# Optimization experiments

Measured on AMD Instinct MI355X. Metric: run time of the kernel, lower is better.

The kernel has to match this reference:

```python
import jax, jax.numpy as jnp
import numpy as np

N, IN_SZ, OUT_SZ = 8192, 512, 64

def setup_inputs() -> dict:
    key = jax.random.key(0)
    ks = jax.random.split(key, 7)
    s_in = 1.0 / np.sqrt(IN_SZ)
    inp = {
        "input": jax.random.normal(ks[0], (N, IN_SZ), dtype=jnp.float32),
        "Wq": jax.random.uniform(ks[1], (OUT_SZ, IN_SZ), jnp.float32, -s_in, s_in),
        "bq": jax.random.uniform(ks[2], (OUT_SZ,), jnp.float32, -s_in, s_in),
        "Wk": jax.random.uniform(ks[3], (OUT_SZ, IN_SZ), jnp.float32, -s_in, s_in),
        "bk": jax.random.uniform(ks[4], (OUT_SZ,), jnp.float32, -s_in, s_in),
        "Wv": jax.random.uniform(ks[5], (OUT_SZ, IN_SZ), jnp.float32, -s_in, s_in),
        "bv": jax.random.uniform(ks[6], (OUT_SZ,), jnp.float32, -s_in, s_in),
    }
    return inp

def reference(input, Wq, bq, Wk, bk, Wv, bv):
    # torch nn.Linear: x @ W.T + b
    q = input @ Wq.T + bq  # [N, out]
    k = input @ Wk.T + bk  # [N, out]
    v = input @ Wv.T + bv  # [N, out]
    # NOTE: original module has NO 1/sqrt(d) scaling.
    scores = jax.nn.softmax(q @ k.T, axis=-1)  # [N, N]
    return scores @ v  # [N, out]
```

## Files before the change

### kernel.cpp

```cpp
#include <hip/hip_runtime.h>
#include <math.h>

#define SA_N   8192
#define SA_IN  512
#define SA_D   64
#define G_SPL  16
#define LOG2E  1.44269504f

typedef short s16x8 __attribute__((ext_vector_type(8)));
typedef float f32x16 __attribute__((ext_vector_type(16)));

#define MFMA32(A, B, C) __builtin_amdgcn_mfma_f32_32x32x16_bf16((A), (B), (C), 0, 0, 0)

static __device__ __forceinline__ unsigned short f2bf_rn(float x) {
    unsigned int u = __float_as_uint(x);
    unsigned int r = (u + 0x7FFFu + ((u >> 16) & 1u)) >> 16;
    return (unsigned short)r;
}

static __device__ __forceinline__ void trunc_split(float f, unsigned short* hi, unsigned short* lo) {
    unsigned int u = __float_as_uint(f);
    *hi = (unsigned short)(u >> 16);
    float lf = f - __uint_as_float(u & 0xFFFF0000u);
    *lo = (unsigned short)(__float_as_uint(lf) >> 16);
}

static __device__ __forceinline__ unsigned int pack_hi16(unsigned int u0, unsigned int u1) {
    return __builtin_amdgcn_perm(u1, u0, 0x07060302u);
}

static __device__ __forceinline__ void split8(const float4 a, const float4 b, s16x8* xh, s16x8* xl) {
    union { unsigned int u[4]; s16x8 v; } H, L;
    const float f[8] = {a.x, a.y, a.z, a.w, b.x, b.y, b.z, b.w};
#pragma unroll
    for (int p = 0; p < 4; ++p) {
        const unsigned int u0 = __float_as_uint(f[2 * p]);
        const unsigned int u1 = __float_as_uint(f[2 * p + 1]);
        H.u[p] = pack_hi16(u0, u1);
        const float l0 = f[2 * p]     - __uint_as_float(u0 & 0xFFFF0000u);
        const float l1 = f[2 * p + 1] - __uint_as_float(u1 & 0xFFFF0000u);
        L.u[p] = pack_hi16(__float_as_uint(l0), __float_as_uint(l1));
    }
    *xh = H.v; *xl = L.v;
}

__global__ __launch_bounds__(256) void prep_w_kernel(
    const float* __restrict__ Wq, const float* __restrict__ Wk, const float* __restrict__ Wv,
    unsigned short* __restrict__ WqH, unsigned short* __restrict__ WqL,
    unsigned short* __restrict__ WkH, unsigned short* __restrict__ WkL,
    unsigned short* __restrict__ WvR)
{
    const int i   = blockIdx.x * 256 + threadIdx.x;
    const int mat = i >> 13;
    const int j   = i & 8191;
    const float4 v = (mat == 0 ? (const float4*)Wq
                    : mat == 1 ? (const float4*)Wk
                               : (const float4*)Wv)[j];
    const float f[4] = {v.x, v.y, v.z, v.w};
    if (mat < 2) {
        unsigned short hs[4], ls[4];
#pragma unroll
        for (int e = 0; e < 4; ++e) trunc_split(f[e], &hs[e], &ls[e]);
        ushort4 H = {hs[0], hs[1], hs[2], hs[3]};
        ushort4 L = {ls[0], ls[1], ls[2], ls[3]};
        unsigned short* WH = mat ? WkH : WqH;
        unsigned short* WL = mat ? WkL : WqL;
        *(ushort4*)(WH + (size_t)j * 4) = H;
        *(ushort4*)(WL + (size_t)j * 4) = L;
    } else {
        ushort4 R = {f2bf_rn(f[0]), f2bf_rn(f[1]), f2bf_rn(f[2]), f2bf_rn(f[3])};
        *(ushort4*)(WvR + (size_t)j * 4) = R;
    }
}

__global__ __launch_bounds__(256, 2) void qkv_kernel(
    const float* __restrict__ in,
    const unsigned short* __restrict__ WqH, const unsigned short* __restrict__ WqL,
    const unsigned short* __restrict__ WkH, const unsigned short* __restrict__ WkL,
    const unsigned short* __restrict__ WvR,
    const float* __restrict__ bq, const float* __restrict__ bk, const float* __restrict__ bv,
    unsigned short* __restrict__ Qhi, unsigned short* __restrict__ Qlo,
    unsigned short* __restrict__ KhiF, unsigned short* __restrict__ VF)
{
    __shared__ float cbuf[2][4][64][20];
    __shared__ __align__(16) unsigned short stage[4096];
    const int t    = threadIdx.x;
    const int w    = t >> 6;
    const int lane = t & 63;
    const int h    = lane >> 5;
    const int q32  = lane & 31;
    const int mat  = blockIdx.x >> 8;
    const int jt   = blockIdx.x & 255;
    const int rows0 = jt * 32;

    const unsigned short* WH = (mat == 0) ? WqH : (mat == 1 ? WkH : WvR);
    const unsigned short* WL = (mat == 0) ? WqL : WkL;
    const float* B = (mat == 0) ? bq : (mat == 1 ? bk : bv);

    f32x16 accA[2] = {};
    f32x16 accB[2] = {};

#pragma unroll 2
    for (int ksl = 0; ksl < 8; ++ksl) {
        const int ks = (w << 3) + ksl;
        const float* xp = in + (size_t)(rows0 + q32) * SA_IN + ks * 16 + h * 8;
        const float4 xa = *(const float4*)xp;
        const float4 xb = *(const float4*)(xp + 4);
        s16x8 xh, xl;
        split8(xa, xb, &xh, &xl);
#pragma unroll
        for (int mt = 0; mt < 2; ++mt) {
            const size_t woff = (size_t)(mt * 32 + q32) * SA_IN + ks * 16 + h * 8;
            const s16x8 ah = *(const s16x8*)(WH + woff);
            if (mat < 2) {
                const s16x8 al = *(const s16x8*)(WL + woff);
                accA[mt] = MFMA32(ah, xh, accA[mt]);
                accB[mt] = MFMA32(ah, xl, accB[mt]);
                accA[mt] = MFMA32(al, xh, accA[mt]);
            } else {
                accA[mt] = MFMA32(ah, xh, accA[mt]);
            }
        }
    }

#pragma unroll
    for (int mt = 0; mt < 2; ++mt) {
        f32x16 tot = accA[mt];
        if (mat < 2) {
#pragma unroll
            for (int r = 0; r < 16; ++r) tot[r] += accB[mt][r];
        }
#pragma unroll
        for (int rg = 0; rg < 4; ++rg) {
            float4 vv = { tot[4 * rg + 0], tot[4 * rg + 1],
                          tot[4 * rg + 2], tot[4 * rg + 3] };
            *(float4*)&cbuf[mt][w][lane][4 * rg] = vv;
        }
    }
    __syncthreads();
    if (w < 2) {
        const int mt = w;
        float c[16];
#pragma unroll
        for (int rg = 0; rg < 4; ++rg) {
            const float4 s0 = *(const float4*)&cbuf[mt][0][lane][4 * rg];
            const float4 s1 = *(const float4*)&cbuf[mt][1][lane][4 * rg];
            const float4 s2 = *(const float4*)&cbuf[mt][2][lane][4 * rg];
            const float4 s3 = *(const float4*)&cbuf[mt][3][lane][4 * rg];
            c[4 * rg + 0] = (s0.x + s1.x) + (s2.x + s3.x);
            c[4 * rg + 1] = (s0.y + s1.y) + (s2.y + s3.y);
            c[4 * rg + 2] = (s0.z + s1.z) + (s2.z + s3.z);
            c[4 * rg + 3] = (s0.w + s1.w) + (s2.w + s3.w);
        }
#pragma unroll
        for (int r = 0; r < 16; ++r) {
            const int o = mt * 32 + (r & 3) + 8 * (r >> 2) + 4 * h;
            float val = c[r] + B[o];
            if (mat == 0) {
                val *= LOG2E;
                unsigned short hi, lo;
                trunc_split(val, &hi, &lo);
                stage[q32 * 64 + o]        = hi;
                stage[2048 + q32 * 64 + o] = lo;
            } else if (mat == 1) {
                const int kl_ = ((o >> 4) * 64 + ((o >> 3) & 1) * 32 + q32) * 8 + (o & 7);
                stage[kl_] = f2bf_rn(val);
            } else {
                const int hp = (q32 >> 2) & 1;
                const int ip = (q32 & 3) + ((q32 >> 3) & 1) * 4;
                const int vl_ = ((o >> 5) * 2 + (q32 >> 4)) * 512
                              + hp * 256 + (o & 31) * 8 + ip;
                stage[vl_] = f2bf_rn(val);
            }
        }
    }
    __syncthreads();

    {
        const uint4* st4 = (const uint4*)stage;
        if (mat == 0) {
            for (int i = t; i < 512; i += 256) {
                unsigned short* dst = ((i < 256) ? Qhi : Qlo) + (size_t)rows0 * 64 + (i & 255) * 8;
                *(uint4*)dst = st4[i];
            }
        } else if (mat == 1) {
            if (t < 256) *(uint4*)(KhiF + (size_t)jt * 2048 + t * 8) = st4[t];
        } else {
            *(uint4*)(VF + (size_t)jt * 2048 + t * 8) = st4[t];
        }
    }
}

__global__ __launch_bounds__(512, 2) void attn_kernel(
    const unsigned short* __restrict__ Qhi, const unsigned short* __restrict__ Qlo,
    const unsigned short* __restrict__ KhiF, const unsigned short* __restrict__ VF,
    unsigned short* __restrict__ Opart, float* __restrict__ Lpart)
{
    __shared__ __align__(16) unsigned short kbuf[2][2][2048];
    const int t    = threadIdx.x;
    const int w    = t >> 6;
    const int lane = t & 63;
    const int h    = lane >> 5;
    const int q32  = lane & 31;
    const int qb   = blockIdx.x >> 4;
    const int g    = blockIdx.x & 15;
    const int q0   = (qb * 8 + w) * 32;
    const int jt0  = g * 16;

    const int half = t >> 8;
    const int ti   = t & 255;

    s16x8 qh[4], ql[4];
#pragma unroll
    for (int s = 0; s < 4; ++s) {
        const size_t off = (size_t)(q0 + q32) * 64 + s * 16 + h * 8;
        qh[s] = *reinterpret_cast<const s16x8*>(Qhi + off);
        ql[s] = *reinterpret_cast<const s16x8*>(Qlo + off);
    }

    const unsigned short* SRC = half ? VF : KhiF;

    {
        const uint4 a = *(const uint4*)(SRC + (size_t)jt0 * 2048 + ti * 8);
        *(uint4*)&kbuf[0][half][ti * 8] = a;
    }
    __syncthreads();

    f32x16 O0 = {}, O1 = {};
    float lsum = 0.f;

    for (int it = 0; it < 16; ++it) {
        const int p = it & 1;

        uint4 na;
        if (it < 15) {
            na = *(const uint4*)(SRC + (size_t)(jt0 + it + 1) * 2048 + ti * 8);
        }

        s16x8 kh[4], vv[4];
#pragma unroll
        for (int s = 0; s < 4; ++s) {
            kh[s] = *(const s16x8*)&kbuf[p][0][(s * 64 + lane) * 8];
            vv[s] = *(const s16x8*)&kbuf[p][1][(s * 64 + lane) * 8];
        }

        f32x16 Sa = {}, Sb = {};
        __builtin_amdgcn_s_setprio(1);
#pragma unroll
        for (int s = 0; s < 4; ++s) {
            Sa = MFMA32(kh[s], qh[s], Sa);
            Sb = MFMA32(kh[s], ql[s], Sb);
        }
        __builtin_amdgcn_s_setprio(0);

        float e[16];
#pragma unroll
        for (int r = 0; r < 16; ++r) e[r] = __builtin_amdgcn_exp2f(Sa[r] + Sb[r]);
        lsum += (((e[0] + e[1]) + (e[2] + e[3])) + ((e[4] + e[5]) + (e[6] + e[7])))
              + (((e[8] + e[9]) + (e[10] + e[11])) + ((e[12] + e[13]) + (e[14] + e[15])));

        union { unsigned int u[4]; s16x8 v; } P0, P1;
#pragma unroll
        for (int j2 = 0; j2 < 4; ++j2) {
            P0.u[j2] = pack_hi16(__float_as_uint(e[2 * j2]),     __float_as_uint(e[2 * j2 + 1]));
            P1.u[j2] = pack_hi16(__float_as_uint(e[8 + 2 * j2]), __float_as_uint(e[8 + 2 * j2 + 1]));
        }

        __builtin_amdgcn_s_setprio(1);
        O0 = MFMA32(vv[0], P0.v, O0);
        O0 = MFMA32(vv[1], P1.v, O0);
        O1 = MFMA32(vv[2], P0.v, O1);
        O1 = MFMA32(vv[3], P1.v, O1);
        __builtin_amdgcn_s_setprio(0);

        if (it < 15) {
            *(uint4*)&kbuf[1 - p][half][ti * 8] = na;
        }
        __syncthreads();
    }

    lsum += __shfl_xor(lsum, 32, 64);

    const size_t qg = (size_t)g * SA_N + q0 + q32;
#pragma unroll
    for (int rg = 0; rg < 4; ++rg) {
        const int d0 = 8 * rg + 4 * h;
        uint2 s0, s1;
        s0.x = (unsigned int)f2bf_rn(O0[4 * rg + 0]) | ((unsigned int)f2bf_rn(O0[4 * rg + 1]) << 16);
        s0.y = (unsigned int)f2bf_rn(O0[4 * rg + 2]) | ((unsigned int)f2bf_rn(O0[4 * rg + 3]) << 16);
        s1.x = (unsigned int)f2bf_rn(O1[4 * rg + 0]) | ((unsigned int)f2bf_rn(O1[4 * rg + 1]) << 16);
        s1.y = (unsigned int)f2bf_rn(O1[4 * rg + 2]) | ((unsigned int)f2bf_rn(O1[4 * rg + 3]) << 16);
        *(uint2*)(Opart + qg * 64 + d0)      = s0;
        *(uint2*)(Opart + qg * 64 + d0 + 32) = s1;
    }
    if (h == 0) Lpart[qg] = lsum;
}

__global__ __launch_bounds__(256) void combine_kernel(
    const unsigned short* __restrict__ Opart, const float* __restrict__ Lpart,
    float* __restrict__ out)
{
    const int tid = blockIdx.x * 256 + threadIdx.x;
    const int q  = tid >> 5;
    const int dp = tid & 31;
    const unsigned int* OP = (const unsigned int*)Opart;
    float s0 = 0.f, s1 = 0.f, lt = 0.f;
#pragma unroll
    for (int g = 0; g < G_SPL; ++g) {
        const unsigned int v = OP[((size_t)g * SA_N + q) * 32 + dp];
        s0 += __uint_as_float(v << 16);
        s1 += __uint_as_float(v & 0xFFFF0000u);
        lt += Lpart[(size_t)g * SA_N + q];
    }
    float2 r = { s0 / lt, s1 / lt };
    *(float2*)&out[(size_t)q * 64 + dp * 2] = r;
}

extern "C" void kernel_launch(void* const* d_in, const int* in_sizes, int n_in,
                              void* d_out, int out_size, void* d_ws, size_t ws_size,
                              hipStream_t stream) {
    const float* input = (const float*)d_in[0];
    const float* Wq    = (const float*)d_in[1];
    const float* bq    = (const float*)d_in[2];
    const float* Wk    = (const float*)d_in[3];
    const float* bk    = (const float*)d_in[4];
    const float* Wv    = (const float*)d_in[5];
    const float* bv    = (const float*)d_in[6];
    float* out = (float*)d_out;

    const size_t SEG = (size_t)SA_N * 64;
    unsigned short* Qhi  = (unsigned short*)d_ws;
    unsigned short* Qlo  = Qhi  + SEG;
    unsigned short* KhiF = Qlo  + SEG;
    unsigned short* VF   = KhiF + SEG;
    unsigned short* Opart = VF  + SEG;
    float*          Lpart = (float*)(Opart + (size_t)G_SPL * SA_N * 64);
    unsigned short* WqH = (unsigned short*)(Lpart + (size_t)G_SPL * SA_N);
    unsigned short* WqL = WqH + 32768;
    unsigned short* WkH = WqL + 32768;
    unsigned short* WkL = WkH + 32768;
    unsigned short* WvR = WkL + 32768;

    prep_w_kernel<<<96, 256, 0, stream>>>(Wq, Wk, Wv, WqH, WqL, WkH, WkL, WvR);
    qkv_kernel<<<768, 256, 0, stream>>>(input, WqH, WqL, WkH, WkL, WvR,
                                        bq, bk, bv, Qhi, Qlo, KhiF, VF);
    attn_kernel<<<32 * G_SPL, 512, 0, stream>>>(Qhi, Qlo, KhiF, VF, Opart, Lpart);
    combine_kernel<<<1024, 256, 0, stream>>>(Opart, Lpart, out);
}
```

Measured before the change: 128.2 us.

## Pre-split input to bf16 hi/lo once and retile QKV projection to 64-row tiles

The input matrix is now converted to bf16 hi/lo halves once in the prep kernel and written to workspace, so the QKV kernel no longer re-reads fp32 input and re-splits it for each of the three matrices. The QKV kernel is retiled so each block covers 64 rows, with each wave owning one 32x32 output tile over the full K dimension. This removes the cross-wave split-K reduction through shared memory and one barrier. In exchange it adds a full write and read of an 8 MB split-input buffer, halves the QKV grid, and gives each wave a longer serial K loop.

Result: slower. 140.8 us (+9.8%).

```diff
diff --git a/kernel.cpp b/kernel.cpp
--- a/kernel.cpp
+++ b/kernel.cpp
@@ -29,52 +29,56 @@
     return __builtin_amdgcn_perm(u1, u0, 0x07060302u);
 }
 
-static __device__ __forceinline__ void split8(const float4 a, const float4 b, s16x8* xh, s16x8* xl) {
-    union { unsigned int u[4]; s16x8 v; } H, L;
-    const float f[8] = {a.x, a.y, a.z, a.w, b.x, b.y, b.z, b.w};
-#pragma unroll
-    for (int p = 0; p < 4; ++p) {
-        const unsigned int u0 = __float_as_uint(f[2 * p]);
-        const unsigned int u1 = __float_as_uint(f[2 * p + 1]);
-        H.u[p] = pack_hi16(u0, u1);
-        const float l0 = f[2 * p]     - __uint_as_float(u0 & 0xFFFF0000u);
-        const float l1 = f[2 * p + 1] - __uint_as_float(u1 & 0xFFFF0000u);
-        L.u[p] = pack_hi16(__float_as_uint(l0), __float_as_uint(l1));
-    }
-    *xh = H.v; *xl = L.v;
-}
-
-__global__ __launch_bounds__(256) void prep_w_kernel(
+__global__ __launch_bounds__(256) void prep_kernel(
+    const float* __restrict__ in,
     const float* __restrict__ Wq, const float* __restrict__ Wk, const float* __restrict__ Wv,
+    unsigned short* __restrict__ Xhi, unsigned short* __restrict__ Xlo,
     unsigned short* __restrict__ WqH, unsigned short* __restrict__ WqL,
     unsigned short* __restrict__ WkH, unsigned short* __restrict__ WkL,
     unsigned short* __restrict__ WvR)
 {
-    const int i   = blockIdx.x * 256 + threadIdx.x;
-    const int mat = i >> 13;
-    const int j   = i & 8191;
-    const float4 v = (mat == 0 ? (const float4*)Wq
-                    : mat == 1 ? (const float4*)Wk
-                               : (const float4*)Wv)[j];
-    const float f[4] = {v.x, v.y, v.z, v.w};
-    if (mat < 2) {
-        unsigned short hs[4], ls[4];
-#pragma unroll
-        for (int e = 0; e < 4; ++e) trunc_split(f[e], &hs[e], &ls[e]);
-        ushort4 H = {hs[0], hs[1], hs[2], hs[3]};
-        ushort4 L = {ls[0], ls[1], ls[2], ls[3]};
-        unsigned short* WH = mat ? WkH : WqH;
-        unsigned short* WL = mat ? WkL : WqL;
-        *(ushort4*)(WH + (size_t)j * 4) = H;
-        *(ushort4*)(WL + (size_t)j * 4) = L;
+    const int b = blockIdx.x;
+    if (b < 1024) {
+        const int base = (b * 256 + threadIdx.x) * 4;
+        const float4* src = (const float4*)in;
+#pragma unroll
+        for (int j = 0; j < 4; ++j) {
+            const float4 v = src[base + j];
+            ushort4 H, L;
+            trunc_split(v.x, &H.x, &L.x);
+            trunc_split(v.y, &H.y, &L.y);
+            trunc_split(v.z, &H.z, &L.z);
+            trunc_split(v.w, &H.w, &L.w);
+            ((ushort4*)Xhi)[base + j] = H;
+            ((ushort4*)Xlo)[base + j] = L;
+        }
     } else {
-        ushort4 R = {f2bf_rn(f[0]), f2bf_rn(f[1]), f2bf_rn(f[2]), f2bf_rn(f[3])};
-        *(ushort4*)(WvR + (size_t)j * 4) = R;
+        const int i   = (b - 1024) * 256 + threadIdx.x;
+        const int mat = i >> 13;
+        const int j   = i & 8191;
+        const float4 v = (mat == 0 ? (const float4*)Wq
+                        : mat == 1 ? (const float4*)Wk
+                                   : (const float4*)Wv)[j];
+        const float f[4] = {v.x, v.y, v.z, v.w};
+        if (mat < 2) {
+            unsigned short hs[4], ls[4];
+#pragma unroll
+            for (int e = 0; e < 4; ++e) trunc_split(f[e], &hs[e], &ls[e]);
+            ushort4 H = {hs[0], hs[1], hs[2], hs[3]};
+            ushort4 L = {ls[0], ls[1], ls[2], ls[3]};
+            unsigned short* WH = mat ? WkH : WqH;
+            unsigned short* WL = mat ? WkL : WqL;
+            *(ushort4*)(WH + (size_t)j * 4) = H;
+            *(ushort4*)(WL + (size_t)j * 4) = L;
+        } else {
+            ushort4 R = {f2bf_rn(f[0]), f2bf_rn(f[1]), f2bf_rn(f[2]), f2bf_rn(f[3])};
+            *(ushort4*)(WvR + (size_t)j * 4) = R;
+        }
     }
 }
 
 __global__ __launch_bounds__(256, 2) void qkv_kernel(
-    const float* __restrict__ in,
+    const unsigned short* __restrict__ Xhi, const unsigned short* __restrict__ Xlo,
     const unsigned short* __restrict__ WqH, const unsigned short* __restrict__ WqL,
     const unsigned short* __restrict__ WkH, const unsigned short* __restrict__ WkL,
     const unsigned short* __restrict__ WvR,
@@ -82,96 +86,67 @@
     unsigned short* __restrict__ Qhi, unsigned short* __restrict__ Qlo,
     unsigned short* __restrict__ KhiF, unsigned short* __restrict__ VF)
 {
-    __shared__ float cbuf[2][4][64][20];
-    __shared__ __align__(16) unsigned short stage[4096];
+    __shared__ __align__(16) unsigned short stage[8192];
     const int t    = threadIdx.x;
     const int w    = t >> 6;
     const int lane = t & 63;
     const int h    = lane >> 5;
     const int q32  = lane & 31;
-    const int mat  = blockIdx.x >> 8;
-    const int jt   = blockIdx.x & 255;
-    const int rows0 = jt * 32;
+    const int wr   = w >> 1;
+    const int wc   = w & 1;
+    const int mat  = blockIdx.x >> 7;
+    const int rt   = blockIdx.x & 127;
+    const int rows0 = rt * 64;
 
     const unsigned short* WH = (mat == 0) ? WqH : (mat == 1 ? WkH : WvR);
     const unsigned short* WL = (mat == 0) ? WqL : WkL;
     const float* B = (mat == 0) ? bq : (mat == 1 ? bk : bv);
 
-    f32x16 accA[2] = {};
-    f32x16 accB[2] = {};
-
-#pragma unroll 2
-    for (int ksl = 0; ksl < 8; ++ksl) {
-        const int ks = (w << 3) + ksl;
-        const float* xp = in + (size_t)(rows0 + q32) * SA_IN + ks * 16 + h * 8;
-        const float4 xa = *(const float4*)xp;
-        const float4 xb = *(const float4*)(xp + 4);
-        s16x8 xh, xl;
-        split8(xa, xb, &xh, &xl);
-#pragma unroll
-        for (int mt = 0; mt < 2; ++mt) {
-            const size_t woff = (size_t)(mt * 32 + q32) * SA_IN + ks * 16 + h * 8;
-            const s16x8 ah = *(const s16x8*)(WH + woff);
-            if (mat < 2) {
-                const s16x8 al = *(const s16x8*)(WL + woff);
-                accA[mt] = MFMA32(ah, xh, accA[mt]);
-                accB[mt] = MFMA32(ah, xl, accB[mt]);
-                accA[mt] = MFMA32(al, xh, accA[mt]);
-            } else {
-                accA[mt] = MFMA32(ah, xh, accA[mt]);
-            }
-        }
-    }
-
-#pragma unroll
-    for (int mt = 0; mt < 2; ++mt) {
-        f32x16 tot = accA[mt];
-        if (mat < 2) {
-#pragma unroll
-            for (int r = 0; r < 16; ++r) tot[r] += accB[mt][r];
-        }
-#pragma unroll
-        for (int rg = 0; rg < 4; ++rg) {
-            float4 vv = { tot[4 * rg + 0], tot[4 * rg + 1],
-                          tot[4 * rg + 2], tot[4 * rg + 3] };
-            *(float4*)&cbuf[mt][w][lane][4 * rg] = vv;
-        }
-    }
-    __syncthreads();
-    if (w < 2) {
-        const int mt = w;
-        float c[16];
-#pragma unroll
-        for (int rg = 0; rg < 4; ++rg) {
-            const float4 s0 = *(const float4*)&cbuf[mt][0][lane][4 * rg];
-            const float4 s1 = *(const float4*)&cbuf[mt][1][lane][4 * rg];
-            const float4 s2 = *(const float4*)&cbuf[mt][2][lane][4 * rg];
-            const float4 s3 = *(const float4*)&cbuf[mt][3][lane][4 * rg];
-            c[4 * rg + 0] = (s0.x + s1.x) + (s2.x + s3.x);
-            c[4 * rg + 1] = (s0.y + s1.y) + (s2.y + s3.y);
-            c[4 * rg + 2] = (s0.z + s1.z) + (s2.z + s3.z);
-            c[4 * rg + 3] = (s0.w + s1.w) + (s2.w + s3.w);
-        }
-#pragma unroll
-        for (int r = 0; r < 16; ++r) {
-            const int o = mt * 32 + (r & 3) + 8 * (r >> 2) + 4 * h;
-            float val = c[r] + B[o];
-            if (mat == 0) {
-                val *= LOG2E;
-                unsigned short hi, lo;
-                trunc_split(val, &hi, &lo);
-                stage[q32 * 64 + o]        = hi;
-                stage[2048 + q32 * 64 + o] = lo;
-            } else if (mat == 1) {
-                const int kl_ = ((o >> 4) * 64 + ((o >> 3) & 1) * 32 + q32) * 8 + (o & 7);
-                stage[kl_] = f2bf_rn(val);
-            } else {
-                const int hp = (q32 >> 2) & 1;
-                const int ip = (q32 & 3) + ((q32 >> 3) & 1) * 4;
-                const int vl_ = ((o >> 5) * 2 + (q32 >> 4)) * 512
-                              + hp * 256 + (o & 31) * 8 + ip;
-                stage[vl_] = f2bf_rn(val);
-            }
+    const unsigned short* xh_p = Xhi + (size_t)(rows0 + wr * 32 + q32) * SA_IN + h * 8;
+    const unsigned short* xl_p = Xlo + (size_t)(rows0 + wr * 32 + q32) * SA_IN + h * 8;
+    const unsigned short* wh_p = WH  + (size_t)(wc * 32 + q32) * SA_IN + h * 8;
+    const unsigned short* wl_p = WL  + (size_t)(wc * 32 + q32) * SA_IN + h * 8;
+
+    f32x16 accA = {}, accB = {};
+    if (mat < 2) {
+#pragma unroll 4
+        for (int ks = 0; ks < 32; ++ks) {
+            const s16x8 xh = *(const s16x8*)(xh_p + ks * 16);
+            const s16x8 xl = *(const s16x8*)(xl_p + ks * 16);
+            const s16x8 ah = *(const s16x8*)(wh_p + ks * 16);
+            const s16x8 al = *(const s16x8*)(wl_p + ks * 16);
+            accA = MFMA32(ah, xh, accA);
+            accB = MFMA32(ah, xl, accB);
+            accA = MFMA32(al, xh, accA);
+        }
+    } else {
+#pragma unroll 4
+        for (int ks = 0; ks < 32; ++ks) {
+            const s16x8 xh = *(const s16x8*)(xh_p + ks * 16);
+            const s16x8 ah = *(const s16x8*)(wh_p + ks * 16);
+            accA = MFMA32(ah, xh, accA);
+        }
+    }
+
+#pragma unroll
+    for (int r = 0; r < 16; ++r) {
+        const int o = wc * 32 + (r & 3) + 8 * (r >> 2) + 4 * h;
+        float val = accA[r] + (mat < 2 ? accB[r] : 0.f) + B[o];
+        if (mat == 0) {
+            val *= LOG2E;
+            unsigned short hi, lo;
+            trunc_split(val, &hi, &lo);
+            stage[(wr * 32 + q32) * 64 + o]        = hi;
+            stage[4096 + (wr * 32 + q32) * 64 + o] = lo;
+        } else if (mat == 1) {
+            const int kl_ = ((o >> 4) * 64 + ((o >> 3) & 1) * 32 + q32) * 8 + (o & 7);
+            stage[wr * 2048 + kl_] = f2bf_rn(val);
+        } else {
+            const int hp = (q32 >> 2) & 1;
+            const int ip = (q32 & 3) + ((q32 >> 3) & 1) * 4;
+            const int vl_ = ((o >> 5) * 2 + (q32 >> 4)) * 512
+                          + hp * 256 + (o & 31) * 8 + ip;
+            stage[wr * 2048 + vl_] = f2bf_rn(val);
         }
     }
     __syncthreads();
@@ -179,14 +154,25 @@
     {
         const uint4* st4 = (const uint4*)stage;
         if (mat == 0) {
-            for (int i = t; i < 512; i += 256) {
-                unsigned short* dst = ((i < 256) ? Qhi : Qlo) + (size_t)rows0 * 64 + (i & 255) * 8;
+#pragma unroll
+            for (int j = 0; j < 4; ++j) {
+                const int i = t + j * 256;
+                unsigned short* dst = (i < 512 ? Qhi + (size_t)rows0 * 64 + i * 8
+                                               : Qlo + (size_t)rows0 * 64 + (i - 512) * 8);
                 *(uint4*)dst = st4[i];
             }
         } else if (mat == 1) {
-            if (t < 256) *(uint4*)(KhiF + (size_t)jt * 2048 + t * 8) = st4[t];
+#pragma unroll
+            for (int j = 0; j < 2; ++j) {
+                const int i = t + j * 256;
+                *(uint4*)(KhiF + (size_t)rows0 * 64 + i * 8) = st4[i];
+            }
         } else {
-            *(uint4*)(VF + (size_t)jt * 2048 + t * 8) = st4[t];
+#pragma unroll
+            for (int j = 0; j < 2; ++j) {
+                const int i = t + j * 256;
+                *(uint4*)(VF + (size_t)rows0 * 64 + i * 8) = st4[i];
+            }
         }
     }
 }
@@ -340,9 +326,12 @@
     unsigned short* WkH = WqL + 32768;
     unsigned short* WkL = WkH + 32768;
     unsigned short* WvR = WkL + 32768;
-
-    prep_w_kernel<<<96, 256, 0, stream>>>(Wq, Wk, Wv, WqH, WqL, WkH, WkL, WvR);
-    qkv_kernel<<<768, 256, 0, stream>>>(input, WqH, WqL, WkH, WkL, WvR,
+    unsigned short* Xhi = WvR + 32768;
+    unsigned short* Xlo = Xhi + (size_t)SA_N * SA_IN;
+
+    prep_kernel<<<1120, 256, 0, stream>>>(input, Wq, Wk, Wv, Xhi, Xlo,
+                                          WqH, WqL, WkH, WkL, WvR);
+    qkv_kernel<<<384, 256, 0, stream>>>(Xhi, Xlo, WqH, WqL, WkH, WkL, WvR,
                                         bq, bk, bv, Qhi, Qlo, KhiF, VF);
     attn_kernel<<<32 * G_SPL, 512, 0, stream>>>(Qhi, Qlo, KhiF, VF, Opart, Lpart);
     combine_kernel<<<1024, 256, 0, stream>>>(Opart, Lpart, out);
```
